# Optimization experiments

Hardware: AMD Instinct MI355X
Metric: run time of the kernel (lower is better)

## Reference

```python
import jax, jax.numpy as jnp
import numpy as np

N = 20000      # nodes
E = 320000     # edges
DIN = 128
DOUT = 10
H = 1024
HM = 256
EPS = 1e-5


def setup_inputs() -> dict:
    key = jax.random.key(0)
    ks = jax.random.split(key, 16)
    sc = 0.02
    return {
        "x": jax.random.normal(ks[0], (N, DIN), dtype=jnp.float32),
        "edge_index": jax.random.randint(ks[1], (2, E), 0, N, dtype=jnp.int64),
        "edge_weight": jax.random.uniform(ks[2], (E,), dtype=jnp.float32),
        "W1": jax.random.normal(ks[3], (DIN, H), dtype=jnp.float32) * sc,
        "b1": jnp.zeros((H,), jnp.float32),
        "g1": jnp.ones((H,), jnp.float32),
        "beta1": jnp.zeros((H,), jnp.float32),
        "W2": jax.random.normal(ks[4], (H, H), dtype=jnp.float32) * sc,
        "b2": jnp.zeros((H,), jnp.float32),
        "g2": jnp.ones((H,), jnp.float32),
        "beta2": jnp.zeros((H,), jnp.float32),
        "Wl1": jax.random.normal(ks[5], (H, HM), dtype=jnp.float32) * sc,
        "bl1": jnp.zeros((HM,), jnp.float32),
        "Wl2": jax.random.normal(ks[6], (HM, DOUT), dtype=jnp.float32) * sc,
        "bl2": jnp.zeros((DOUT,), jnp.float32),
    }


def _gcn_conv(x, W, b, src, dst, w):
    # PyG GCNConv: linear transform, symmetric normalization (self-loops
    # already appended to src/dst/w), scatter-add aggregation at dst.
    h = x @ W                                        # [N, out]
    deg = jax.ops.segment_sum(w, dst, num_segments=N)
    dinv = jnp.where(deg > 0, jax.lax.rsqrt(deg), 0.0)
    norm = dinv[src] * w * dinv[dst]                 # [E+N]
    agg = jax.ops.segment_sum(norm[:, None] * h[src], dst, num_segments=N)
    return agg + b


def _batchnorm(x, g, b):
    m = x.mean(axis=0)
    v = jnp.mean(jnp.square(x - m), axis=0)          # biased var (torch BN)
    return g * (x - m) * jax.lax.rsqrt(v + EPS) + b


def reference(x, edge_index, edge_weight,
              W1, b1, g1, beta1, W2, b2, g2, beta2,
              Wl1, bl1, Wl2, bl2):
    loop = jnp.arange(N, dtype=edge_index.dtype)
    src = jnp.concatenate([edge_index[0], loop])
    dst = jnp.concatenate([edge_index[1], loop])
    w = jnp.concatenate([edge_weight, jnp.ones((N,), edge_weight.dtype)])

    h = jax.nn.relu(_batchnorm(_gcn_conv(x, W1, b1, src, dst, w), g1, beta1))
    h = jax.nn.relu(_batchnorm(_gcn_conv(h, W2, b2, src, dst, w), g2, beta2))
    h = jax.nn.relu(h @ Wl1 + bl1) @ Wl2 + bl2
    return jax.nn.log_softmax(h, axis=1)
```

## Files before the change

kernel.cpp:

```cpp
#include <hip/hip_runtime.h>
#include <math.h>

static constexpr int Nn  = 20000;
static constexpr int Ne  = 320000;
static constexpr int DIN = 128;
static constexpr int DOUTc = 10;
static constexpr int Hc  = 1024;
static constexpr int HMc = 256;
static constexpr float EPSc = 1e-5f;

typedef __bf16 bf16_t;
typedef __bf16 bf16x8 __attribute__((ext_vector_type(8)));
typedef __bf16 bf16x4 __attribute__((ext_vector_type(4)));
typedef float  f32x4  __attribute__((ext_vector_type(4)));

__device__ __forceinline__ void gload_lds16(const bf16_t* g, bf16_t* lds) {
    __builtin_amdgcn_global_load_lds(
        (const __attribute__((address_space(1))) void*)g,
        (__attribute__((address_space(3))) void*)lds, 16, 0, 0);
}

__global__ __launch_bounds__(256) void deg_init_k(float* __restrict__ deg, int* __restrict__ cnt) {
    int i = blockIdx.x * 256 + threadIdx.x;
    if (i < Nn) { deg[i] = 1.0f; cnt[i] = 0; }
}

__global__ __launch_bounds__(256)
void deg_edge_k(const float* __restrict__ w, const int* __restrict__ dstv,
                float* __restrict__ deg, int* __restrict__ cnt) {
    int e = blockIdx.x * 256 + threadIdx.x;
    if (e < Ne) {
        int d = dstv[e];
        atomicAdd(&deg[d], w[e]);
        atomicAdd(&cnt[d], 1);
    }
}

__global__ __launch_bounds__(256) void dinv_k(float* __restrict__ deg) {
    int i = blockIdx.x * 256 + threadIdx.x;
    if (i < Nn) deg[i] = rsqrtf(deg[i]);
}

__global__ __launch_bounds__(1024)
void scan_k(const int* __restrict__ cnt, int* __restrict__ row_ptr, int* __restrict__ cursor)
{
    __shared__ int wsum[16];
    __shared__ int tot_s;
    __shared__ int carry_s;
    const int tid  = threadIdx.x;
    const int lane = tid & 63;
    const int wv   = tid >> 6;
    if (tid == 0) carry_s = 0;
    __syncthreads();
    for (int base = 0; base < Nn; base += 1024) {
        int i = base + tid;
        int v = (i < Nn) ? cnt[i] : 0;
        int s = v;
        #pragma unroll
        for (int off = 1; off < 64; off <<= 1) {
            int t = __shfl_up(s, off, 64);
            if (lane >= off) s += t;
        }
        if (lane == 63) wsum[wv] = s;
        __syncthreads();
        if (tid < 16) {
            int t = wsum[tid];
            int s2v = t;
            #pragma unroll
            for (int off = 1; off < 16; off <<= 1) {
                int u = __shfl_up(s2v, off, 64);
                if (tid >= off) s2v += u;
            }
            wsum[tid] = s2v - t;
            if (tid == 15) tot_s = s2v;
        }
        __syncthreads();
        int carry = carry_s;
        if (i < Nn) {
            int excl = carry + wsum[wv] + s - v;
            row_ptr[i] = excl;
            cursor[i]  = excl;
        }
        __syncthreads();
        if (tid == 0) carry_s = carry + tot_s;
        __syncthreads();
    }
    if (tid == 0) row_ptr[Nn] = Ne;
}

__global__ __launch_bounds__(256)
void csr_fill_k(const int* __restrict__ srcv, const int* __restrict__ dstv,
                const float* __restrict__ w, const float* __restrict__ dinv,
                int* __restrict__ cursor, int* __restrict__ csr_src,
                float* __restrict__ csr_coeff)
{
    int e = blockIdx.x * 256 + threadIdx.x;
    if (e >= Ne) return;
    int s = srcv[e], d = dstv[e];
    int pos = atomicAdd(&cursor[d], 1);
    csr_src[pos]   = s;
    csr_coeff[pos] = dinv[s] * w[e] * dinv[d];
}

__global__ __launch_bounds__(256)
void spmm_x_k(const bf16x8* __restrict__ x8, const int* __restrict__ row_ptr,
              const int* __restrict__ csr_src, const float* __restrict__ csr_coeff,
              const float* __restrict__ dinv, bf16x8* __restrict__ out8)
{
    int d = blockIdx.x * 16 + (threadIdx.x >> 4);
    int f = threadIdx.x & 15;
    float c = dinv[d]; c = c * c;
    bf16x8 hv = x8[(size_t)d * 16 + f];
    float acc[8];
    #pragma unroll
    for (int i = 0; i < 8; ++i) acc[i] = c * (float)hv[i];
    int beg = row_ptr[d], end = row_ptr[d + 1];
    for (int j = beg; j < end; ++j) {
        int   s  = csr_src[j];
        float cf = csr_coeff[j];
        bf16x8 v = x8[(size_t)s * 16 + f];
        #pragma unroll
        for (int i = 0; i < 8; ++i) acc[i] = fmaf(cf, (float)v[i], acc[i]);
    }
    bf16x8 o;
    #pragma unroll
    for (int i = 0; i < 8; ++i) o[i] = (bf16_t)acc[i];
    out8[(size_t)d * 16 + f] = o;
}

__global__ __launch_bounds__(256)
void spmm_h_k(const bf16x8* __restrict__ h8, const int* __restrict__ row_ptr,
              const int* __restrict__ csr_src, const float* __restrict__ csr_coeff,
              const float* __restrict__ dinv, bf16x8* __restrict__ out8)
{
    int d = blockIdx.x * 2 + (threadIdx.x >> 7);
    int f = threadIdx.x & 127;
    float c = dinv[d]; c = c * c;
    bf16x8 hv = h8[(size_t)d * 128 + f];
    float acc[8];
    #pragma unroll
    for (int i = 0; i < 8; ++i) acc[i] = c * (float)hv[i];
    int beg = row_ptr[d], end = row_ptr[d + 1];
    for (int j = beg; j < end; ++j) {
        int   s  = csr_src[j];
        float cf = csr_coeff[j];
        bf16x8 v = h8[(size_t)s * 128 + f];
        #pragma unroll
        for (int i = 0; i < 8; ++i) acc[i] = fmaf(cf, (float)v[i], acc[i]);
    }
    bf16x8 o;
    #pragma unroll
    for (int i = 0; i < 8; ++i) o[i] = (bf16_t)acc[i];
    out8[(size_t)d * 128 + f] = o;
}

template<int RK, int CN>
__global__ __launch_bounds__(256)
void transpose_bf16_k(const float* __restrict__ W, bf16_t* __restrict__ Wt)
{
    __shared__ float tile[32][33];
    int bx = blockIdx.x * 32;
    int by = blockIdx.y * 32;
    int tx = threadIdx.x & 31, ty = threadIdx.x >> 5;
    #pragma unroll
    for (int p = 0; p < 32; p += 8)
        tile[ty + p][tx] = W[(size_t)(by + ty + p) * CN + bx + tx];
    __syncthreads();
    #pragma unroll
    for (int p = 0; p < 32; p += 8)
        Wt[(size_t)(bx + ty + p) * RK + by + tx] = (bf16_t)tile[tx][ty + p];
}

__global__ __launch_bounds__(256)
void cvt_bf16_k(const float4* __restrict__ in, bf16x4* __restrict__ out, int n4)
{
    int i = blockIdx.x * 256 + threadIdx.x;
    if (i >= n4) return;
    float4 v = in[i];
    bf16x4 o = { (bf16_t)v.x, (bf16_t)v.y, (bf16_t)v.z, (bf16_t)v.w };
    out[i] = o;
}

template<int NC, int KD, bool BIAS, bool RELU, bool OUTBF, bool STATS>
__global__ __launch_bounds__(256)
void gemm_bf16_k(const bf16_t* __restrict__ A, const bf16_t* __restrict__ Bt,
                 const float* __restrict__ bias, void* __restrict__ Cv, int M,
                 float* __restrict__ s1g, float* __restrict__ s2g)
{
    __shared__ __align__(16) bf16_t Asm[128 * 32];
    __shared__ __align__(16) bf16_t Bsm[128 * 32];
    const int tid  = threadIdx.x;
    const int w    = tid >> 6;
    const int lane = tid & 63;
    const int bm = blockIdx.y * 128, bn = blockIdx.x * 128;
    const int l15 = lane & 15, quad = lane >> 4;
    const int wm = (w & 1) * 64, wn = (w >> 1) * 64;
    const int swz = quad ^ ((l15 >> 1) & 3);

    const int srow = lane >> 2;
    const int scol = 8 * ((lane & 3) ^ ((lane >> 3) & 3));
    const int c0 = w * 32;
    int ga0 = bm + c0 + srow;       if (ga0 >= M) ga0 = M - 1;
    int ga1 = bm + c0 + 16 + srow;  if (ga1 >= M) ga1 = M - 1;
    const bf16_t* gA0 = A + (size_t)ga0 * KD + scol;
    const bf16_t* gA1 = A + (size_t)ga1 * KD + scol;
    const bf16_t* gB0 = Bt + (size_t)(bn + c0 + srow) * KD + scol;
    const bf16_t* gB1 = gB0 + (size_t)16 * KD;
    bf16_t* lA0 = Asm + (c0 +  0) * 32;
    bf16_t* lA1 = Asm + (c0 + 16) * 32;
    bf16_t* lB0 = Bsm + (c0 +  0) * 32;
    bf16_t* lB1 = Bsm + (c0 + 16) * 32;

    const bf16_t* pA = Asm + (wm + l15) * 32 + swz * 8;
    const bf16_t* pB = Bsm + (wn + l15) * 32 + swz * 8;

    f32x4 acc[4][4] = {};

    for (int k0 = 0; k0 < KD; k0 += 32) {
        gload_lds16(gA0 + k0, lA0);
        gload_lds16(gA1 + k0, lA1);
        gload_lds16(gB0 + k0, lB0);
        gload_lds16(gB1 + k0, lB1);
        __syncthreads();
        bf16x8 af[4], bfr[4];
        #pragma unroll
        for (int t = 0; t < 4; ++t) {
            af[t]  = *(const bf16x8*)(pA + t * 16 * 32);
            bfr[t] = *(const bf16x8*)(pB + t * 16 * 32);
        }
        #pragma unroll
        for (int mt = 0; mt < 4; ++mt)
            #pragma unroll
            for (int nt = 0; nt < 4; ++nt)
                acc[mt][nt] = __builtin_amdgcn_mfma_f32_16x16x32_bf16(
                    af[mt], bfr[nt], acc[mt][nt], 0, 0, 0);
        __syncthreads();
    }

    #pragma unroll
    for (int mt = 0; mt < 4; ++mt) {
        #pragma unroll
        for (int r = 0; r < 4; ++r) {
            int row = bm + wm + mt * 16 + quad * 4 + r;
            if (row >= M) continue;
            #pragma unroll
            for (int nt = 0; nt < 4; ++nt) {
                int col = bn + wn + nt * 16 + l15;
                float v = acc[mt][nt][r];
                if (BIAS) v += bias[col];
                if (RELU) v = fmaxf(v, 0.f);
                if (OUTBF) ((bf16_t*)Cv)[(size_t)row * NC + col] = (bf16_t)v;
                else       ((float*)Cv)[(size_t)row * NC + col] = v;
            }
        }
    }

    if (STATS) {
        #pragma unroll
        for (int nt = 0; nt < 4; ++nt) {
            float ps = 0.f, pq = 0.f;
            #pragma unroll
            for (int mt = 0; mt < 4; ++mt)
                #pragma unroll
                for (int r = 0; r < 4; ++r) {
                    int row = bm + wm + mt * 16 + quad * 4 + r;
                    if (row < M) {
                        float v = acc[mt][nt][r];
                        ps += v;
                        pq = fmaf(v, v, pq);
                    }
                }
            ps += __shfl_down(ps, 32, 64); ps += __shfl_down(ps, 16, 64);
            pq += __shfl_down(pq, 32, 64); pq += __shfl_down(pq, 16, 64);
            if (quad == 0) {
                int col = bn + wn + nt * 16 + l15;
                atomicAdd(&s1g[col], ps);
                atomicAdd(&s2g[col], pq);
            }
        }
    }
}

__global__ __launch_bounds__(256) void zero_stats_k(float* __restrict__ s) {
    int i = blockIdx.x * 256 + threadIdx.x;
    s[i] = 0.f;
}

__global__ __launch_bounds__(256)
void bn_stats_k(const bf16_t* __restrict__ x, float* __restrict__ s1, float* __restrict__ s2)
{
    int c = blockIdx.x * 256 + threadIdx.x;
    int r0 = blockIdx.y * 250;
    float s = 0.f, q = 0.f;
    const bf16_t* p = x + (size_t)r0 * Hc + c;
    for (int r = 0; r < 250; ++r) {
        float v = (float)p[(size_t)r * Hc];
        s += v;
        q = fmaf(v, v, q);
    }
    atomicAdd(&s1[c], s);
    atomicAdd(&s2[c], q);
}

__global__ __launch_bounds__(256)
void bn_apply_k(const bf16x8* __restrict__ x8, const float* __restrict__ s1,
                const float* __restrict__ s2, const float* __restrict__ g,
                const float* __restrict__ beta, bf16x8* __restrict__ out8)
{
    int idx = blockIdx.x * 256 + threadIdx.x;
    int c8 = (idx & 127) << 3;
    bf16x8 v = x8[idx];
    bf16x8 o;
    #pragma unroll
    for (int i = 0; i < 8; ++i) {
        int c = c8 + i;
        float mean = s1[c] * (1.0f / Nn);
        float var  = s2[c] * (1.0f / Nn) - mean * mean;
        float sc = g[c] * rsqrtf(var + EPSc);
        float sh = beta[c] - mean * sc;
        o[i] = (bf16_t)fmaxf(fmaf((float)v[i], sc, sh), 0.f);
    }
    out8[idx] = o;
}

__global__ __launch_bounds__(256)
void head_k(const float* __restrict__ z, const float* __restrict__ Wl2,
            const float* __restrict__ bl2, float* __restrict__ out)
{
    int wave = threadIdx.x >> 6;
    int lane = threadIdx.x & 63;
    int node = blockIdx.x * 4 + wave;
    const float4 zv = *(const float4*)(z + (size_t)node * HMc + lane * 4);
    float p[DOUTc];
    #pragma unroll
    for (int j = 0; j < DOUTc; ++j) p[j] = 0.f;
    const float zz[4] = {zv.x, zv.y, zv.z, zv.w};
    #pragma unroll
    for (int i = 0; i < 4; ++i) {
        int k = lane * 4 + i;
        const float* wrow = Wl2 + (size_t)k * DOUTc;
        #pragma unroll
        for (int j = 0; j < DOUTc; ++j) p[j] = fmaf(zz[i], wrow[j], p[j]);
    }
    #pragma unroll
    for (int j = 0; j < DOUTc; ++j) {
        #pragma unroll
        for (int off = 32; off > 0; off >>= 1) p[j] += __shfl_down(p[j], off, 64);
    }
    if (lane == 0) {
        float v[DOUTc];
        float m = -1e30f;
        #pragma unroll
        for (int j = 0; j < DOUTc; ++j) { v[j] = p[j] + bl2[j]; m = fmaxf(m, v[j]); }
        float s = 0.f;
        #pragma unroll
        for (int j = 0; j < DOUTc; ++j) s += expf(v[j] - m);
        float ls = logf(s) + m;
        #pragma unroll
        for (int j = 0; j < DOUTc; ++j) out[(size_t)node * DOUTc + j] = v[j] - ls;
    }
}

extern "C" void kernel_launch(void* const* d_in, const int* in_sizes, int n_in,
                              void* d_out, int out_size, void* d_ws, size_t ws_size,
                              hipStream_t stream)
{
    (void)in_sizes; (void)n_in; (void)out_size; (void)ws_size;
    const float* x    = (const float*)d_in[0];
    const int*   ei   = (const int*)d_in[1];
    const float* ew   = (const float*)d_in[2];
    const float* W1   = (const float*)d_in[3];
    const float* gam1 = (const float*)d_in[5];
    const float* bet1 = (const float*)d_in[6];
    const float* W2   = (const float*)d_in[7];
    const float* gam2 = (const float*)d_in[9];
    const float* bet2 = (const float*)d_in[10];
    const float* Wl1  = (const float*)d_in[11];
    const float* bl1  = (const float*)d_in[12];
    const float* Wl2  = (const float*)d_in[13];
    const float* bl2  = (const float*)d_in[14];
    float* out = (float*)d_out;

    float* zhead = (float*)d_ws;
    float* dinv  = zhead + (size_t)Nn * HMc;
    float* s1    = dinv + Nn;
    float* s2    = s1 + Hc;
    int*   cnt      = (int*)(s2 + Hc);
    int*   row_ptr  = cnt + Nn;
    int*   cursor   = row_ptr + Nn + 16;
    int*   csr_src  = cursor + Nn;
    float* csr_coef = (float*)(csr_src + Ne);
    bf16_t* xb   = (bf16_t*)(csr_coef + Ne);
    bf16_t* xagg = xb + (size_t)Nn * DIN;
    bf16_t* hgem = xagg + (size_t)Nn * DIN;
    bf16_t* hbf  = hgem + (size_t)Nn * Hc;
    bf16_t* W1t  = hbf + (size_t)Nn * Hc;
    bf16_t* W2t  = W1t + (size_t)Hc * DIN;
    bf16_t* Wl1t = W2t + (size_t)Hc * Hc;

    const int* srcv = ei;
    const int* dstv = ei + Ne;

    deg_init_k<<<(Nn + 255) / 256, 256, 0, stream>>>(dinv, cnt);
    deg_edge_k<<<(Ne + 255) / 256, 256, 0, stream>>>(ew, dstv, dinv, cnt);
    dinv_k<<<(Nn + 255) / 256, 256, 0, stream>>>(dinv);
    scan_k<<<1, 1024, 0, stream>>>(cnt, row_ptr, cursor);
    csr_fill_k<<<(Ne + 255) / 256, 256, 0, stream>>>(srcv, dstv, ew, dinv, cursor,
                                                     csr_src, csr_coef);
    transpose_bf16_k<DIN, Hc><<<dim3(Hc / 32, DIN / 32), 256, 0, stream>>>(W1, W1t);
    transpose_bf16_k<Hc, Hc><<<dim3(Hc / 32, Hc / 32), 256, 0, stream>>>(W2, W2t);
    transpose_bf16_k<Hc, HMc><<<dim3(HMc / 32, Hc / 32), 256, 0, stream>>>(Wl1, Wl1t);
    cvt_bf16_k<<<(Nn * DIN / 4 + 255) / 256, 256, 0, stream>>>(
        (const float4*)x, (bf16x4*)xb, Nn * DIN / 4);

    const int MB = (Nn + 127) / 128;

    spmm_x_k<<<Nn / 16, 256, 0, stream>>>((const bf16x8*)xb, row_ptr, csr_src,
                                          csr_coef, dinv, (bf16x8*)xagg);
    zero_stats_k<<<8, 256, 0, stream>>>(s1);
    gemm_bf16_k<Hc, DIN, false, false, true, true><<<dim3(Hc / 128, MB), 256, 0, stream>>>(
        xagg, W1t, nullptr, hgem, Nn, s1, s2);
    bn_apply_k<<<Nn * Hc / 8 / 256, 256, 0, stream>>>(
        (const bf16x8*)hgem, s1, s2, gam1, bet1, (bf16x8*)hbf);

    gemm_bf16_k<Hc, Hc, false, false, true, false><<<dim3(Hc / 128, MB), 256, 0, stream>>>(
        hbf, W2t, nullptr, hgem, Nn, nullptr, nullptr);
    spmm_h_k<<<Nn / 2, 256, 0, stream>>>((const bf16x8*)hgem, row_ptr, csr_src,
                                         csr_coef, dinv, (bf16x8*)hbf);
    zero_stats_k<<<8, 256, 0, stream>>>(s1);
    bn_stats_k<<<dim3(Hc / 256, 80), 256, 0, stream>>>(hbf, s1, s2);
    bn_apply_k<<<Nn * Hc / 8 / 256, 256, 0, stream>>>(
        (const bf16x8*)hbf, s1, s2, gam2, bet2, (bf16x8*)hgem);

    gemm_bf16_k<HMc, Hc, true, true, false, false><<<dim3(HMc / 128, MB), 256, 0, stream>>>(
        hgem, Wl1t, bl1, zhead, Nn, nullptr, nullptr);
    head_k<<<Nn / 4, 256, 0, stream>>>(zhead, Wl2, bl2, out);
}
```

Before: 477.0 us.

## Parallelize CSR scan across blocks and split SpMM by feature panels

Replaces the single-block serial scan with a three-kernel block-parallel scan (per-block scan, block-offset scan, offset add). Also reorganizes both SpMM kernels so each block handles many nodes over a narrow feature panel instead of a few nodes over all features. The panel split is meant to give more independent rows per block and better cache locality for the gathered source rows. It adds two extra kernel launches for the scan and gathers each neighbor list once per panel.

```diff
diff --git a/kernel.cpp b/kernel.cpp
--- a/kernel.cpp
+++ b/kernel.cpp
@@ -8,6 +8,7 @@
 static constexpr int Hc  = 1024;
 static constexpr int HMc = 256;
 static constexpr float EPSc = 1e-5f;
+static constexpr int NB_SCAN = (Nn + 255) / 256;
 
 typedef __bf16 bf16_t;
 typedef __bf16 bf16x8 __attribute__((ext_vector_type(8)));
@@ -41,51 +42,57 @@
     if (i < Nn) deg[i] = rsqrtf(deg[i]);
 }
 
-__global__ __launch_bounds__(1024)
-void scan_k(const int* __restrict__ cnt, int* __restrict__ row_ptr, int* __restrict__ cursor)
-{
-    __shared__ int wsum[16];
-    __shared__ int tot_s;
-    __shared__ int carry_s;
-    const int tid  = threadIdx.x;
-    const int lane = tid & 63;
-    const int wv   = tid >> 6;
-    if (tid == 0) carry_s = 0;
+__global__ __launch_bounds__(256)
+void scanA_k(const int* __restrict__ cnt, int* __restrict__ row_ptr, int* __restrict__ blk)
+{
+    __shared__ int wsum[4];
+    int b = blockIdx.x, tid = threadIdx.x, lane = tid & 63, wv = tid >> 6;
+    int i = b * 256 + tid;
+    int v = (i < Nn) ? cnt[i] : 0;
+    int s = v;
+    #pragma unroll
+    for (int off = 1; off < 64; off <<= 1) {
+        int t = __shfl_up(s, off, 64);
+        if (lane >= off) s += t;
+    }
+    if (lane == 63) wsum[wv] = s;
     __syncthreads();
-    for (int base = 0; base < Nn; base += 1024) {
-        int i = base + tid;
-        int v = (i < Nn) ? cnt[i] : 0;
-        int s = v;
-        #pragma unroll
-        for (int off = 1; off < 64; off <<= 1) {
-            int t = __shfl_up(s, off, 64);
-            if (lane >= off) s += t;
-        }
-        if (lane == 63) wsum[wv] = s;
-        __syncthreads();
-        if (tid < 16) {
-            int t = wsum[tid];
-            int s2v = t;
-            #pragma unroll
-            for (int off = 1; off < 16; off <<= 1) {
-                int u = __shfl_up(s2v, off, 64);
-                if (tid >= off) s2v += u;
-            }
-            wsum[tid] = s2v - t;
-            if (tid == 15) tot_s = s2v;
-        }
-        __syncthreads();
-        int carry = carry_s;
-        if (i < Nn) {
-            int excl = carry + wsum[wv] + s - v;
-            row_ptr[i] = excl;
-            cursor[i]  = excl;
-        }
-        __syncthreads();
-        if (tid == 0) carry_s = carry + tot_s;
-        __syncthreads();
-    }
-    if (tid == 0) row_ptr[Nn] = Ne;
+    int wo = 0;
+    #pragma unroll
+    for (int k = 0; k < 4; ++k) if (k < wv) wo += wsum[k];
+    if (i < Nn) row_ptr[i] = wo + s - v;
+    if (tid == 255) blk[b] = wo + s;
+}
+
+__global__ __launch_bounds__(128)
+void scanB_k(int* __restrict__ blk)
+{
+    __shared__ int w0;
+    int tid = threadIdx.x, lane = tid & 63, wv = tid >> 6;
+    int v = (tid < NB_SCAN) ? blk[tid] : 0;
+    int s = v;
+    #pragma unroll
+    for (int off = 1; off < 64; off <<= 1) {
+        int t = __shfl_up(s, off, 64);
+        if (lane >= off) s += t;
+    }
+    if (tid == 63) w0 = s;
+    __syncthreads();
+    int excl = s - v + (wv ? w0 : 0);
+    if (tid < NB_SCAN) blk[tid] = excl;
+}
+
+__global__ __launch_bounds__(256)
+void scanC_k(int* __restrict__ row_ptr, const int* __restrict__ blk, int* __restrict__ cursor)
+{
+    int b = blockIdx.x;
+    int i = b * 256 + threadIdx.x;
+    if (i < Nn) {
+        int r = row_ptr[i] + blk[b];
+        row_ptr[i] = r;
+        cursor[i]  = r;
+    }
+    if (i == 0) row_ptr[Nn] = Ne;
 }
 
 __global__ __launch_bounds__(256)
@@ -107,14 +114,16 @@
               const int* __restrict__ csr_src, const float* __restrict__ csr_coeff,
               const float* __restrict__ dinv, bf16x8* __restrict__ out8)
 {
-    int d = blockIdx.x * 16 + (threadIdx.x >> 4);
-    int f = threadIdx.x & 15;
-    float c = dinv[d]; c = c * c;
-    bf16x8 hv = x8[(size_t)d * 16 + f];
+    int panel = blockIdx.x & 3;
+    int node  = (blockIdx.x >> 2) * 64 + (threadIdx.x >> 2);
+    if (node >= Nn) return;
+    int f = (threadIdx.x & 3) + panel * 4;
+    float c = dinv[node]; c = c * c;
+    bf16x8 hv = x8[(size_t)node * 16 + f];
     float acc[8];
     #pragma unroll
     for (int i = 0; i < 8; ++i) acc[i] = c * (float)hv[i];
-    int beg = row_ptr[d], end = row_ptr[d + 1];
+    int beg = row_ptr[node], end = row_ptr[node + 1];
     for (int j = beg; j < end; ++j) {
         int   s  = csr_src[j];
         float cf = csr_coeff[j];
@@ -125,7 +134,7 @@
     bf16x8 o;
     #pragma unroll
     for (int i = 0; i < 8; ++i) o[i] = (bf16_t)acc[i];
-    out8[(size_t)d * 16 + f] = o;
+    out8[(size_t)node * 16 + f] = o;
 }
 
 __global__ __launch_bounds__(256)
@@ -133,14 +142,15 @@
               const int* __restrict__ csr_src, const float* __restrict__ csr_coeff,
               const float* __restrict__ dinv, bf16x8* __restrict__ out8)
 {
-    int d = blockIdx.x * 2 + (threadIdx.x >> 7);
-    int f = threadIdx.x & 127;
-    float c = dinv[d]; c = c * c;
-    bf16x8 hv = h8[(size_t)d * 128 + f];
+    int panel = blockIdx.x & 7;
+    int node  = (blockIdx.x >> 3) * 16 + (threadIdx.x >> 4);
+    int f     = (threadIdx.x & 15) + panel * 16;
+    float c = dinv[node]; c = c * c;
+    bf16x8 hv = h8[(size_t)node * 128 + f];
     float acc[8];
     #pragma unroll
     for (int i = 0; i < 8; ++i) acc[i] = c * (float)hv[i];
-    int beg = row_ptr[d], end = row_ptr[d + 1];
+    int beg = row_ptr[node], end = row_ptr[node + 1];
     for (int j = beg; j < end; ++j) {
         int   s  = csr_src[j];
         float cf = csr_coeff[j];
@@ -151,7 +161,7 @@
     bf16x8 o;
     #pragma unroll
     for (int i = 0; i < 8; ++i) o[i] = (bf16_t)acc[i];
-    out8[(size_t)d * 128 + f] = o;
+    out8[(size_t)node * 128 + f] = o;
 }
 
 template<int RK, int CN>
@@ -388,7 +398,8 @@
     int*   cnt      = (int*)(s2 + Hc);
     int*   row_ptr  = cnt + Nn;
     int*   cursor   = row_ptr + Nn + 16;
-    int*   csr_src  = cursor + Nn;
+    int*   blk      = cursor + Nn;
+    int*   csr_src  = blk + 128;
     float* csr_coef = (float*)(csr_src + Ne);
     bf16_t* xb   = (bf16_t*)(csr_coef + Ne);
     bf16_t* xagg = xb + (size_t)Nn * DIN;
@@ -404,7 +415,9 @@
     deg_init_k<<<(Nn + 255) / 256, 256, 0, stream>>>(dinv, cnt);
     deg_edge_k<<<(Ne + 255) / 256, 256, 0, stream>>>(ew, dstv, dinv, cnt);
     dinv_k<<<(Nn + 255) / 256, 256, 0, stream>>>(dinv);
-    scan_k<<<1, 1024, 0, stream>>>(cnt, row_ptr, cursor);
+    scanA_k<<<NB_SCAN, 256, 0, stream>>>(cnt, row_ptr, blk);
+    scanB_k<<<1, 128, 0, stream>>>(blk);
+    scanC_k<<<NB_SCAN, 256, 0, stream>>>(row_ptr, blk, cursor);
     csr_fill_k<<<(Ne + 255) / 256, 256, 0, stream>>>(srcv, dstv, ew, dinv, cursor,
                                                      csr_src, csr_coef);
     transpose_bf16_k<DIN, Hc><<<dim3(Hc / 32, DIN / 32), 256, 0, stream>>>(W1, W1t);
@@ -415,8 +428,8 @@
 
     const int MB = (Nn + 127) / 128;
 
-    spmm_x_k<<<Nn / 16, 256, 0, stream>>>((const bf16x8*)xb, row_ptr, csr_src,
-                                          csr_coef, dinv, (bf16x8*)xagg);
+    spmm_x_k<<<4 * ((Nn + 63) / 64), 256, 0, stream>>>(
+        (const bf16x8*)xb, row_ptr, csr_src, csr_coef, dinv, (bf16x8*)xagg);
     zero_stats_k<<<8, 256, 0, stream>>>(s1);
     gemm_bf16_k<Hc, DIN, false, false, true, true><<<dim3(Hc / 128, MB), 256, 0, stream>>>(
         xagg, W1t, nullptr, hgem, Nn, s1, s2);
@@ -425,8 +438,8 @@
 
     gemm_bf16_k<Hc, Hc, false, false, true, false><<<dim3(Hc / 128, MB), 256, 0, stream>>>(
         hbf, W2t, nullptr, hgem, Nn, nullptr, nullptr);
-    spmm_h_k<<<Nn / 2, 256, 0, stream>>>((const bf16x8*)hgem, row_ptr, csr_src,
-                                         csr_coef, dinv, (bf16x8*)hbf);
+    spmm_h_k<<<8 * (Nn / 16), 256, 0, stream>>>(
+        (const bf16x8*)hgem, row_ptr, csr_src, csr_coef, dinv, (bf16x8*)hbf);
     zero_stats_k<<<8, 256, 0, stream>>>(s1);
     bn_stats_k<<<dim3(Hc / 256, 80), 256, 0, stream>>>(hbf, s1, s2);
     bn_apply_k<<<Nn * Hc / 8 / 256, 256, 0, stream>>>(
```

Result: faster. 461.9 us (-3.2%).
